# Optimization experiments

Measured on AMD Instinct MI355X. Metric: run time of the kernel, lower is better.

The kernel has to match this reference:

```python
import jax, jax.numpy as jnp
import numpy as np
import math

H = 16  # n_head
DK = 64  # d_k = n_feat // n_head
BASE = 10000.0


def _rope_cos_sin(T, dk, dtype):
    inv_freq = 1.0 / (BASE ** (jnp.arange(0, dk, 2, dtype=jnp.float32) / dk))
    t = jnp.arange(T, dtype=jnp.float32)
    freqs = jnp.einsum('i,j->ij', t, inv_freq)          # [T, dk/2]
    emb = jnp.concatenate([freqs, freqs], axis=-1)       # [T, dk]
    return jnp.cos(emb).astype(dtype)[:, None, None, :], jnp.sin(emb).astype(dtype)[:, None, None, :]


def _rotate_half(x):
    x1, x2 = jnp.split(x, 2, axis=-1)
    return jnp.concatenate([-x2, x1], axis=-1)


def setup_inputs() -> dict:
    key = jax.random.key(0)
    ks = jax.random.split(key, 8)
    T, B, C = 2048, 2, 1024
    s = 0.02
    return {
        'query': jax.random.normal(ks[0], (T, B, C), jnp.float32),
        'key': jax.random.normal(ks[1], (T, B, C), jnp.float32),
        'value': jax.random.normal(ks[2], (T, B, C), jnp.float32),
        'Wq': jax.random.normal(ks[3], (C, C), jnp.float32) * s,
        'bq': jnp.zeros((C,), jnp.float32),
        'Wk': jax.random.normal(ks[4], (C, C), jnp.float32) * s,
        'bk': jnp.zeros((C,), jnp.float32),
        'Wv': jax.random.normal(ks[5], (C, C), jnp.float32) * s,
        'bv': jnp.zeros((C,), jnp.float32),
        'Wo': jax.random.normal(ks[6], (C, C), jnp.float32) * s,
        'bo': jnp.zeros((C,), jnp.float32),
    }


def reference(query, key, value, Wq, bq, Wk, bk, Wv, bv, Wo, bo):
    T, B, C = value.shape
    # --- RoPE applied to raw inputs (per the original module), before projections ---
    q = query.reshape(T, B, H, DK)
    k = key.reshape(T, B, H, DK)
    cos, sin = _rope_cos_sin(T, DK, q.dtype)  # [T,1,1,DK]
    q = q * cos + _rotate_half(q) * sin
    k = k * cos + _rotate_half(k) * sin
    q = q.reshape(T, B, C).transpose(1, 0, 2)   # [B,T,C]
    k = k.reshape(T, B, C).transpose(1, 0, 2)
    v = value.transpose(1, 0, 2)
    # --- QKV projections (torch Linear: x @ W.T + b) ---
    q = (jnp.einsum('btc,dc->btd', q, Wq) + bq).reshape(B, T, H, DK).transpose(0, 2, 1, 3)
    k = (jnp.einsum('btc,dc->btd', k, Wk) + bk).reshape(B, T, H, DK).transpose(0, 2, 1, 3)
    v = (jnp.einsum('btc,dc->btd', v, Wv) + bv).reshape(B, T, H, DK).transpose(0, 2, 1, 3)
    # --- scaled dot-product attention ---
    scores = jnp.einsum('bhqd,bhkd->bhqk', q, k) / math.sqrt(DK)
    attn = jax.nn.softmax(scores, axis=-1)
    x = jnp.einsum('bhqk,bhkd->bhqd', attn, v)        # [B,H,T,DK]
    x = x.transpose(0, 2, 1, 3).reshape(B, T, C)
    out = jnp.einsum('btc,dc->btd', x, Wo) + bo        # [B,T,C]
    return out.transpose(1, 0, 2)                      # [T,B,C]
```

## Files before the change

kernel.cpp:

```cpp
#include <hip/hip_runtime.h>
#include <hip/hip_bf16.h>
#include <math.h>

#define T_SEQ 2048
#define B_SZ 2
#define C_DIM 1024
#define H_HEADS 16
#define DKH 64
#define M_ROWS (T_SEQ * B_SZ)

#define QSCALE 0.1803368801111204f

typedef __attribute__((ext_vector_type(8))) short bf16x8;
typedef __attribute__((ext_vector_type(4))) float f32x4;
typedef unsigned short ushort_t;


__device__ __forceinline__ ushort_t f2bf(float f) {
    unsigned u = __float_as_uint(f);
    u += 0x7fffu + ((u >> 16) & 1u);
    return (ushort_t)(u >> 16);
}
__device__ __forceinline__ unsigned pack2bf(float a, float b) {
    return (unsigned)f2bf(a) | ((unsigned)f2bf(b) << 16);
}

__device__ __forceinline__ void async_copy16(const void* g, void* l) {
    __builtin_amdgcn_global_load_lds(
        (const __attribute__((address_space(1))) void*)g,
        (__attribute__((address_space(3))) void*)l, 16, 0, 0);
}

__global__ __launch_bounds__(256) void rope_cast_qk(
        const float* __restrict__ q, const float* __restrict__ k,
        ushort_t* __restrict__ qb, ushort_t* __restrict__ kb) {
    int idx  = blockIdx.x * 256 + threadIdx.x;
    int j    = idx & 31;
    int rest = idx >> 5;
    int h    = rest & (H_HEADS - 1);
    int tb   = rest >> 4;
    int t    = tb >> 1;
    float inv = exp2f(-(float)j * 0.41524101186092034f);
    float ang = (float)t * inv;
    float s, c;
    sincosf(ang, &s, &c);
    int base = tb * C_DIM + h * DKH + j;
    float q1 = q[base], q2 = q[base + 32];
    float k1 = k[base], k2 = k[base + 32];
    qb[base]      = f2bf(q1 * c - q2 * s);
    qb[base + 32] = f2bf(q2 * c + q1 * s);
    kb[base]      = f2bf(k1 * c - k2 * s);
    kb[base + 32] = f2bf(k2 * c + k1 * s);
}

__global__ __launch_bounds__(256) void cast_bf16(
        const float* __restrict__ in, ushort_t* __restrict__ out, int n4) {
    int i = blockIdx.x * 256 + threadIdx.x;
    if (i < n4) {
        float4 v = reinterpret_cast<const float4*>(in)[i];
        ushort4 o;
        o.x = f2bf(v.x); o.y = f2bf(v.y); o.z = f2bf(v.z); o.w = f2bf(v.w);
        reinterpret_cast<ushort4*>(out)[i] = o;
    }
}

__global__ __launch_bounds__(256) void cast_value_perm(
        const float* __restrict__ in, ushort_t* __restrict__ out) {
    int i   = blockIdx.x * 256 + threadIdx.x;
    int c4  = i & 255;
    int row = i >> 8;
    int b   = row >> 11, t = row & 2047;
    float4 v = reinterpret_cast<const float4*>(in)[(t * 2 + b) * 256 + c4];
    ushort4 o;
    o.x = f2bf(v.x); o.y = f2bf(v.y); o.z = f2bf(v.z); o.w = f2bf(v.w);
    reinterpret_cast<ushort4*>(out)[i] = o;
}

template <bool BF16_OUT, bool BIAS_ROW>
__global__ __launch_bounds__(256) void gemm_nt(
        const ushort_t* __restrict__ A, const ushort_t* __restrict__ W,
        const float* __restrict__ bias, void* __restrict__ Cout,
        int M, int N, int K, float scale) {
    __shared__ ushort_t As[128 * 64];
    __shared__ ushort_t Bs[128 * 64];
    const int tid  = threadIdx.x;
    const int lane = tid & 63;
    const int w    = tid >> 6;
    const int wr   = w >> 1, wc = w & 1;
    const int m16  = lane & 15, quad = lane >> 4;
    const int r8   = lane >> 3, c8 = lane & 7;
    const int clog = c8 ^ r8;
    const int rowBase = blockIdx.y * 128;
    const int colBase = blockIdx.x * 128;

    f32x4 acc[4][4];
#pragma unroll
    for (int i = 0; i < 4; i++)
#pragma unroll
        for (int j = 0; j < 4; j++) acc[i][j] = (f32x4){0.f, 0.f, 0.f, 0.f};

    for (int kt = 0; kt < K; kt += 64) {
        __syncthreads();
#pragma unroll
        for (int i = 0; i < 4; ++i) {
            int R = w * 32 + i * 8;
            async_copy16(A + (size_t)(rowBase + R + r8) * K + kt + clog * 8,
                         &As[R * 64]);
            async_copy16(W + (size_t)(colBase + R + r8) * K + kt + clog * 8,
                         &Bs[R * 64]);
        }
        __syncthreads();
#pragma unroll
        for (int ks = 0; ks < 2; ++ks) {
            bf16x8 af[4], bfr[4];
            int lc = ks * 4 + quad;
#pragma unroll
            for (int mi = 0; mi < 4; mi++) {
                int R = wr * 64 + mi * 16 + m16;
                af[mi] = *reinterpret_cast<const bf16x8*>(
                    &As[R * 64 + ((lc ^ (R & 7)) << 3)]);
            }
#pragma unroll
            for (int ni = 0; ni < 4; ni++) {
                int R = wc * 64 + ni * 16 + m16;
                bfr[ni] = *reinterpret_cast<const bf16x8*>(
                    &Bs[R * 64 + ((lc ^ (R & 7)) << 3)]);
            }
#pragma unroll
            for (int mi = 0; mi < 4; mi++)
#pragma unroll
                for (int ni = 0; ni < 4; ni++)
                    acc[mi][ni] = __builtin_amdgcn_mfma_f32_16x16x32_bf16(
                        af[mi], bfr[ni], acc[mi][ni], 0, 0, 0);
        }
    }
#pragma unroll
    for (int mi = 0; mi < 4; mi++)
#pragma unroll
        for (int ni = 0; ni < 4; ni++)
#pragma unroll
            for (int r = 0; r < 4; r++) {
                int row = rowBase + wr * 64 + mi * 16 + quad * 4 + r;
                int col = colBase + wc * 64 + ni * 16 + m16;
                float v = (acc[mi][ni][r] + (BIAS_ROW ? bias[row] : bias[col])) * scale;
                if (BF16_OUT)
                    ((ushort_t*)Cout)[(size_t)row * N + col] = f2bf(v);
                else
                    ((float*)Cout)[(size_t)row * N + col] = v;
            }
}

__global__ __launch_bounds__(256) void attn(
        const ushort_t* __restrict__ Qp, const ushort_t* __restrict__ Kp,
        const ushort_t* __restrict__ VTg, ushort_t* __restrict__ X) {
    __shared__ ushort_t Qt[64 * 64];
    __shared__ ushort_t Kt[2][64 * 64];
    __shared__ ushort_t VT[2][64 * 64];

    const int tid  = threadIdx.x;
    const int lane = tid & 63;
    const int w    = tid >> 6;
    const int m16  = lane & 15, quad = lane >> 4;
    const int r8   = lane >> 3, c8 = lane & 7;
    const int clog = c8 ^ r8;

    const int lid   = blockIdx.x + blockIdx.y * 32;
    const int jj    = lid >> 3;
    const int pair  = (lid & 7) * 4 + (jj >> 5);
    const int qBase = (jj & 31) * 64;
    const int b = pair >> 4, h = pair & 15;

#pragma unroll
    for (int i = 0; i < 2; ++i) {
        int R = w * 16 + i * 8;
        async_copy16(Qp + (size_t)((qBase + R + r8) * 2 + b) * C_DIM + h * DKH + clog * 8,
                     &Qt[R * 64]);
    }
    __syncthreads();
    bf16x8 aq[2];
#pragma unroll
    for (int ks = 0; ks < 2; ks++) {
        int R = w * 16 + m16;
        aq[ks] = *reinterpret_cast<const bf16x8*>(
            &Qt[R * 64 + (((ks * 4 + quad) ^ (m16 & 7)) << 3)]);
    }
    asm volatile("s_waitcnt lgkmcnt(0)" ::: "memory");
    __syncthreads();

    ushort_t* Pw = &Qt[w * 16 * 64];

    float lrun = 0.f;
    f32x4 o[4];
#pragma unroll
    for (int mi = 0; mi < 4; mi++) o[mi] = (f32x4){0.f, 0.f, 0.f, 0.f};

    for (int kt = 0; kt < T_SEQ; kt += 128) {
        __syncthreads();
#pragma unroll
        for (int half = 0; half < 2; ++half) {
            int key0 = kt + half * 64;
#pragma unroll
            for (int i = 0; i < 2; ++i) {
                int R = w * 16 + i * 8;
                async_copy16(Kp + (size_t)((key0 + R + r8) * 2 + b) * C_DIM + h * DKH + clog * 8,
                             &Kt[half][R * 64]);
                async_copy16(VTg + (size_t)(h * DKH + R + r8) * M_ROWS + b * T_SEQ + key0 + clog * 8,
                             &VT[half][R * 64]);
            }
        }
        __syncthreads();

#pragma unroll
        for (int half = 0; half < 2; ++half) {
            f32x4 s[4];
#pragma unroll
            for (int ni = 0; ni < 4; ni++) s[ni] = (f32x4){0.f, 0.f, 0.f, 0.f};
#pragma unroll
            for (int ks = 0; ks < 2; ks++) {
#pragma unroll
                for (int ni = 0; ni < 4; ni++) {
                    int R = ni * 16 + m16;
                    bf16x8 kf = *reinterpret_cast<const bf16x8*>(
                        &Kt[half][R * 64 + (((ks * 4 + quad) ^ (m16 & 7)) << 3)]);
                    s[ni] = __builtin_amdgcn_mfma_f32_16x16x32_bf16(kf, aq[ks], s[ni], 0, 0, 0);
                }
            }

            float p[4][4];
            float rs = 0.f;
#pragma unroll
            for (int ni = 0; ni < 4; ni++)
#pragma unroll
                for (int r = 0; r < 4; r++) {
                    p[ni][r] = __builtin_amdgcn_exp2f(s[ni][r]);
                    rs += p[ni][r];
                }
            lrun += rs;
#pragma unroll
            for (int ni = 0; ni < 4; ni++) {
                uint2 pv;
                pv.x = pack2bf(p[ni][0], p[ni][1]);
                pv.y = pack2bf(p[ni][2], p[ni][3]);
                int chunk = ((ni * 2 + (quad >> 1)) ^ (m16 & 7));
                reinterpret_cast<uint2*>(Pw)[m16 * 16 + chunk * 2 + (quad & 1)] = pv;
            }
            asm volatile("s_waitcnt lgkmcnt(0)" ::: "memory");

#pragma unroll
            for (int ks = 0; ks < 2; ks++) {
                bf16x8 pf = *reinterpret_cast<const bf16x8*>(
                    &Pw[m16 * 64 + (((ks * 4 + quad) ^ (m16 & 7)) << 3)]);
#pragma unroll
                for (int mi = 0; mi < 4; mi++) {
                    int R = mi * 16 + m16;
                    bf16x8 vf = *reinterpret_cast<const bf16x8*>(
                        &VT[half][R * 64 + (((ks * 4 + quad) ^ (m16 & 7)) << 3)]);
                    o[mi] = __builtin_amdgcn_mfma_f32_16x16x32_bf16(vf, pf, o[mi], 0, 0, 0);
                }
            }
        }
    }

    lrun += __shfl_xor(lrun, 16);
    lrun += __shfl_xor(lrun, 32);
    float invl = 1.0f / lrun;

#pragma unroll
    for (int mi = 0; mi < 4; mi++) {
        uint2 ov;
        ov.x = pack2bf(o[mi][0] * invl, o[mi][1] * invl);
        ov.y = pack2bf(o[mi][2] * invl, o[mi][3] * invl);
        int chunk = ((mi * 2 + (quad >> 1)) ^ (m16 & 7));
        reinterpret_cast<uint2*>(Pw)[m16 * 16 + chunk * 2 + (quad & 1)] = ov;
    }
    asm volatile("s_waitcnt lgkmcnt(0)" ::: "memory");
#pragma unroll
    for (int it = 0; it < 2; ++it) {
        int ql = lane >> 2;
        int c  = (lane & 3) + 4 * it;
        bf16x8 vo = *reinterpret_cast<const bf16x8*>(
            &Pw[ql * 64 + ((c ^ (ql & 7)) << 3)]);
        int t = qBase + w * 16 + ql;
        *reinterpret_cast<bf16x8*>(
            &X[(size_t)(t * 2 + b) * C_DIM + h * DKH + c * 8]) = vo;
    }
}

extern "C" void kernel_launch(void* const* d_in, const int* in_sizes, int n_in,
                              void* d_out, int out_size, void* d_ws, size_t ws_size,
                              hipStream_t stream) {
    const float* query = (const float*)d_in[0];
    const float* key   = (const float*)d_in[1];
    const float* value = (const float*)d_in[2];
    const float* Wq = (const float*)d_in[3];
    const float* bq = (const float*)d_in[4];
    const float* Wk = (const float*)d_in[5];
    const float* bk = (const float*)d_in[6];
    const float* Wv = (const float*)d_in[7];
    const float* bv = (const float*)d_in[8];
    const float* Wo = (const float*)d_in[9];
    const float* bo = (const float*)d_in[10];
    float* out = (float*)d_out;

    ushort_t* qb  = (ushort_t*)d_ws;
    ushort_t* kb  = qb  + (size_t)M_ROWS * C_DIM;
    ushort_t* vb2 = kb  + (size_t)M_ROWS * C_DIM;
    ushort_t* Wqb = vb2 + (size_t)M_ROWS * C_DIM;
    ushort_t* Wkb = Wqb + (size_t)C_DIM * C_DIM;
    ushort_t* Wvb = Wkb + (size_t)C_DIM * C_DIM;
    ushort_t* Wob = Wvb + (size_t)C_DIM * C_DIM;
    ushort_t* Qp  = Wob + (size_t)C_DIM * C_DIM;
    ushort_t* Kp  = Qp  + (size_t)M_ROWS * C_DIM;
    ushort_t* VTg = Kp  + (size_t)M_ROWS * C_DIM;
    ushort_t* Xb  = VTg + (size_t)M_ROWS * C_DIM;

    rope_cast_qk<<<(T_SEQ * B_SZ * H_HEADS * 32) / 256, 256, 0, stream>>>(query, key, qb, kb);
    cast_value_perm<<<(M_ROWS * C_DIM / 4) / 256, 256, 0, stream>>>(value, vb2);
    cast_bf16<<<(C_DIM * C_DIM / 4) / 256, 256, 0, stream>>>(Wq, Wqb, C_DIM * C_DIM / 4);
    cast_bf16<<<(C_DIM * C_DIM / 4) / 256, 256, 0, stream>>>(Wk, Wkb, C_DIM * C_DIM / 4);
    cast_bf16<<<(C_DIM * C_DIM / 4) / 256, 256, 0, stream>>>(Wv, Wvb, C_DIM * C_DIM / 4);
    cast_bf16<<<(C_DIM * C_DIM / 4) / 256, 256, 0, stream>>>(Wo, Wob, C_DIM * C_DIM / 4);

    dim3 gg(C_DIM / 128, M_ROWS / 128);
    gemm_nt<true, false><<<gg, 256, 0, stream>>>(qb, Wqb, bq, Qp, M_ROWS, C_DIM, C_DIM, QSCALE);
    gemm_nt<true, false><<<gg, 256, 0, stream>>>(kb, Wkb, bk, Kp, M_ROWS, C_DIM, C_DIM, 1.0f);
    dim3 gv(M_ROWS / 128, C_DIM / 128);
    gemm_nt<true, true><<<gv, 256, 0, stream>>>(Wvb, vb2, bv, VTg, C_DIM, M_ROWS, C_DIM, 1.0f);

    attn<<<dim3(T_SEQ / 64, B_SZ * H_HEADS), 256, 0, stream>>>(Qp, Kp, VTg, Xb);

    gemm_nt<false, false><<<gg, 256, 0, stream>>>(Xb, Wob, bo, (void*)out, M_ROWS, C_DIM, C_DIM, 1.0f);
}
```

Measured before the change: 279.1 us.

## Use 8-wave GEMM blocks, hardware bf16 pack, and precomputed attention LDS offsets

The GEMM kernel now runs 512 threads (8 waves) per 128x128 tile, with each wave owning a 32x64 sub-tile instead of 64x64. This halves per-thread accumulators and gives more waves per block to hide latency. The pack2bf helper uses the hardware packed f32-to-bf16 conversion builtin when it is available. The attention kernel precomputes swizzled byte offsets for the K, V and P LDS accesses to cut address arithmetic in the inner loop. Smaller per-wave tiles raise LDS fragment traffic per MFMA, and the hardware conversion's rounding may differ slightly from the manual round-to-nearest-even.

```diff
diff --git a/kernel.cpp b/kernel.cpp
--- a/kernel.cpp
+++ b/kernel.cpp
@@ -21,8 +21,16 @@
     u += 0x7fffu + ((u >> 16) & 1u);
     return (ushort_t)(u >> 16);
 }
+
 __device__ __forceinline__ unsigned pack2bf(float a, float b) {
+#if __has_builtin(__builtin_amdgcn_cvt_pk_bf16_f32)
+    typedef __attribute__((ext_vector_type(2))) __bf16 bf16x2_t;
+    union { bf16x2_t v; unsigned u; } cv;
+    cv.v = __builtin_amdgcn_cvt_pk_bf16_f32(a, b);
+    return cv.u;
+#else
     return (unsigned)f2bf(a) | ((unsigned)f2bf(b) << 16);
+#endif
 }
 
 __device__ __forceinline__ void async_copy16(const void* g, void* l) {
@@ -77,7 +85,7 @@
 }
 
 template <bool BF16_OUT, bool BIAS_ROW>
-__global__ __launch_bounds__(256) void gemm_nt(
+__global__ __launch_bounds__(512) void gemm_nt(
         const ushort_t* __restrict__ A, const ushort_t* __restrict__ W,
         const float* __restrict__ bias, void* __restrict__ Cout,
         int M, int N, int K, float scale) {
@@ -86,24 +94,25 @@
     const int tid  = threadIdx.x;
     const int lane = tid & 63;
     const int w    = tid >> 6;
-    const int wr   = w >> 1, wc = w & 1;
+    const int wr   = w >> 1;
+    const int wc   = w & 1;
     const int m16  = lane & 15, quad = lane >> 4;
     const int r8   = lane >> 3, c8 = lane & 7;
     const int clog = c8 ^ r8;
     const int rowBase = blockIdx.y * 128;
     const int colBase = blockIdx.x * 128;
 
-    f32x4 acc[4][4];
-#pragma unroll
-    for (int i = 0; i < 4; i++)
+    f32x4 acc[2][4];
+#pragma unroll
+    for (int i = 0; i < 2; i++)
 #pragma unroll
         for (int j = 0; j < 4; j++) acc[i][j] = (f32x4){0.f, 0.f, 0.f, 0.f};
 
     for (int kt = 0; kt < K; kt += 64) {
         __syncthreads();
 #pragma unroll
-        for (int i = 0; i < 4; ++i) {
-            int R = w * 32 + i * 8;
+        for (int i = 0; i < 2; ++i) {
+            int R = w * 16 + i * 8;
             async_copy16(A + (size_t)(rowBase + R + r8) * K + kt + clog * 8,
                          &As[R * 64]);
             async_copy16(W + (size_t)(colBase + R + r8) * K + kt + clog * 8,
@@ -112,11 +121,11 @@
         __syncthreads();
 #pragma unroll
         for (int ks = 0; ks < 2; ++ks) {
-            bf16x8 af[4], bfr[4];
+            bf16x8 af[2], bfr[4];
             int lc = ks * 4 + quad;
 #pragma unroll
-            for (int mi = 0; mi < 4; mi++) {
-                int R = wr * 64 + mi * 16 + m16;
+            for (int mi = 0; mi < 2; mi++) {
+                int R = wr * 32 + mi * 16 + m16;
                 af[mi] = *reinterpret_cast<const bf16x8*>(
                     &As[R * 64 + ((lc ^ (R & 7)) << 3)]);
             }
@@ -127,7 +136,7 @@
                     &Bs[R * 64 + ((lc ^ (R & 7)) << 3)]);
             }
 #pragma unroll
-            for (int mi = 0; mi < 4; mi++)
+            for (int mi = 0; mi < 2; mi++)
 #pragma unroll
                 for (int ni = 0; ni < 4; ni++)
                     acc[mi][ni] = __builtin_amdgcn_mfma_f32_16x16x32_bf16(
@@ -135,12 +144,12 @@
         }
     }
 #pragma unroll
-    for (int mi = 0; mi < 4; mi++)
+    for (int mi = 0; mi < 2; mi++)
 #pragma unroll
         for (int ni = 0; ni < 4; ni++)
 #pragma unroll
             for (int r = 0; r < 4; r++) {
-                int row = rowBase + wr * 64 + mi * 16 + quad * 4 + r;
+                int row = rowBase + wr * 32 + mi * 16 + quad * 4 + r;
                 int col = colBase + wc * 64 + ni * 16 + m16;
                 float v = (acc[mi][ni][r] + (BIAS_ROW ? bias[row] : bias[col])) * scale;
                 if (BF16_OUT)
@@ -170,6 +179,18 @@
     const int qBase = (jj & 31) * 64;
     const int b = pair >> 4, h = pair & 15;
 
+    const int swz0 = (quad ^ (m16 & 7)) << 4;
+    const int swz1 = ((4 + quad) ^ (m16 & 7)) << 4;
+    const int ofA  = m16 * 128 + swz0;
+    const int ofB  = m16 * 128 + swz1;
+    const char* KtC = (const char*)Kt;
+    const char* VTC = (const char*)VT;
+    char*       PwC = (char*)Qt + w * 2048;
+    int pwo[4];
+#pragma unroll
+    for (int ni = 0; ni < 4; ni++)
+        pwo[ni] = m16 * 128 + (((ni * 2 + (quad >> 1)) ^ (m16 & 7)) << 4) + (quad & 1) * 8;
+
 #pragma unroll
     for (int i = 0; i < 2; ++i) {
         int R = w * 16 + i * 8;
@@ -178,16 +199,10 @@
     }
     __syncthreads();
     bf16x8 aq[2];
-#pragma unroll
-    for (int ks = 0; ks < 2; ks++) {
-        int R = w * 16 + m16;
-        aq[ks] = *reinterpret_cast<const bf16x8*>(
-            &Qt[R * 64 + (((ks * 4 + quad) ^ (m16 & 7)) << 3)]);
-    }
+    aq[0] = *reinterpret_cast<const bf16x8*>((const char*)Qt + w * 2048 + ofA);
+    aq[1] = *reinterpret_cast<const bf16x8*>((const char*)Qt + w * 2048 + ofB);
     asm volatile("s_waitcnt lgkmcnt(0)" ::: "memory");
     __syncthreads();
-
-    ushort_t* Pw = &Qt[w * 16 * 64];
 
     float lrun = 0.f;
     f32x4 o[4];
@@ -217,11 +232,11 @@
             for (int ni = 0; ni < 4; ni++) s[ni] = (f32x4){0.f, 0.f, 0.f, 0.f};
 #pragma unroll
             for (int ks = 0; ks < 2; ks++) {
+                const int ofk = ks ? ofB : ofA;
 #pragma unroll
                 for (int ni = 0; ni < 4; ni++) {
-                    int R = ni * 16 + m16;
                     bf16x8 kf = *reinterpret_cast<const bf16x8*>(
-                        &Kt[half][R * 64 + (((ks * 4 + quad) ^ (m16 & 7)) << 3)]);
+                        KtC + half * 8192 + ni * 2048 + ofk);
                     s[ni] = __builtin_amdgcn_mfma_f32_16x16x32_bf16(kf, aq[ks], s[ni], 0, 0, 0);
                 }
             }
@@ -241,20 +256,18 @@
                 uint2 pv;
                 pv.x = pack2bf(p[ni][0], p[ni][1]);
                 pv.y = pack2bf(p[ni][2], p[ni][3]);
-                int chunk = ((ni * 2 + (quad >> 1)) ^ (m16 & 7));
-                reinterpret_cast<uint2*>(Pw)[m16 * 16 + chunk * 2 + (quad & 1)] = pv;
+                *reinterpret_cast<uint2*>(PwC + pwo[ni]) = pv;
             }
             asm volatile("s_waitcnt lgkmcnt(0)" ::: "memory");
 
 #pragma unroll
             for (int ks = 0; ks < 2; ks++) {
-                bf16x8 pf = *reinterpret_cast<const bf16x8*>(
-                    &Pw[m16 * 64 + (((ks * 4 + quad) ^ (m16 & 7)) << 3)]);
+                const int ofk = ks ? ofB : ofA;
+                bf16x8 pf = *reinterpret_cast<const bf16x8*>(PwC + ofk);
 #pragma unroll
                 for (int mi = 0; mi < 4; mi++) {
-                    int R = mi * 16 + m16;
                     bf16x8 vf = *reinterpret_cast<const bf16x8*>(
-                        &VT[half][R * 64 + (((ks * 4 + quad) ^ (m16 & 7)) << 3)]);
+                        VTC + half * 8192 + mi * 2048 + ofk);
                     o[mi] = __builtin_amdgcn_mfma_f32_16x16x32_bf16(vf, pf, o[mi], 0, 0, 0);
                 }
             }
@@ -270,10 +283,10 @@
         uint2 ov;
         ov.x = pack2bf(o[mi][0] * invl, o[mi][1] * invl);
         ov.y = pack2bf(o[mi][2] * invl, o[mi][3] * invl);
-        int chunk = ((mi * 2 + (quad >> 1)) ^ (m16 & 7));
-        reinterpret_cast<uint2*>(Pw)[m16 * 16 + chunk * 2 + (quad & 1)] = ov;
+        *reinterpret_cast<uint2*>(PwC + pwo[mi]) = ov;
     }
     asm volatile("s_waitcnt lgkmcnt(0)" ::: "memory");
+    ushort_t* Pw = (ushort_t*)PwC;
 #pragma unroll
     for (int it = 0; it < 2; ++it) {
         int ql = lane >> 2;
@@ -322,12 +335,12 @@
     cast_bf16<<<(C_DIM * C_DIM / 4) / 256, 256, 0, stream>>>(Wo, Wob, C_DIM * C_DIM / 4);
 
     dim3 gg(C_DIM / 128, M_ROWS / 128);
-    gemm_nt<true, false><<<gg, 256, 0, stream>>>(qb, Wqb, bq, Qp, M_ROWS, C_DIM, C_DIM, QSCALE);
-    gemm_nt<true, false><<<gg, 256, 0, stream>>>(kb, Wkb, bk, Kp, M_ROWS, C_DIM, C_DIM, 1.0f);
+    gemm_nt<true, false><<<gg, 512, 0, stream>>>(qb, Wqb, bq, Qp, M_ROWS, C_DIM, C_DIM, QSCALE);
+    gemm_nt<true, false><<<gg, 512, 0, stream>>>(kb, Wkb, bk, Kp, M_ROWS, C_DIM, C_DIM, 1.0f);
     dim3 gv(M_ROWS / 128, C_DIM / 128);
-    gemm_nt<true, true><<<gv, 256, 0, stream>>>(Wvb, vb2, bv, VTg, C_DIM, M_ROWS, C_DIM, 1.0f);
+    gemm_nt<true, true><<<gv, 512, 0, stream>>>(Wvb, vb2, bv, VTg, C_DIM, M_ROWS, C_DIM, 1.0f);
 
     attn<<<dim3(T_SEQ / 64, B_SZ * H_HEADS), 256, 0, stream>>>(Qp, Kp, VTg, Xb);
 
-    gemm_nt<false, false><<<gg, 256, 0, stream>>>(Xb, Wob, bo, (void*)out, M_ROWS, C_DIM, C_DIM, 1.0f);
-}
+    gemm_nt<false, false><<<gg, 512, 0, stream>>>(Xb, Wob, bo, (void*)out, M_ROWS, C_DIM, C_DIM, 1.0f);
+}
```

Result: faster. 265.2 us (-5.0%).
